# Performance work log

Hardware: AMD Instinct MI355X
Metric: run time of the kernel (lower is better)

The kernel has to match this reference:

```python
import jax, jax.numpy as jnp
import numpy as np

MARGIN = 5.0
NUM_CLASSES = 21


def setup_inputs() -> dict:
    key = jax.random.key(0)
    k1, k2, k3 = jax.random.split(key, 3)
    B, D, C = 65536, 512, NUM_CLASSES
    features = jax.random.normal(k1, (B, D), dtype=jnp.float32)
    centers = jax.random.normal(k2, (C, D), dtype=jnp.float32)
    labels = jax.random.randint(k3, (B,), 0, C, dtype=jnp.int64)
    return {"features": features, "centers": centers, "labels": labels}


def reference(features, centers, labels):
    # Halved squared euclidean distances, batch x num_classes, via the
    # ||f||^2 + ||c||^2 - 2 f.c expansion (avoids a B x C x D intermediate).
    f2 = jnp.sum(features * features, axis=1, keepdims=True)      # (B, 1)
    c2 = jnp.sum(centers * centers, axis=1)[None, :]              # (1, C)
    d = 0.5 * (f2 + c2 - 2.0 * (features @ centers.T))            # (B, C)

    B = features.shape[0]
    pos = d[jnp.arange(B), labels]                                 # dist to own center
    same = labels[:, None] == jnp.arange(NUM_CLASSES)[None, :]     # (B, C)
    neg = jnp.min(jnp.where(same, jnp.inf, d), axis=1)             # nearest other center
    loss = jnp.mean(jax.nn.relu(pos + MARGIN - neg))
    return loss
```

## Files before the change

### kernel.cpp

```cpp
#include <hip/hip_runtime.h>
#include <float.h>

#define DIM      512
#define NCLS     21
#define MARGIN_V 5.0f
#define ROWS_PB  64
#define DC       32
#define NSTAGE   (DIM / DC)
#define LPAD     (DC + 1)

__global__ __launch_bounds__(64)
void center_norm_kernel(const float* __restrict__ centers,
                        float* __restrict__ halfc2) {
    const int c = blockIdx.x;
    const int t = threadIdx.x;
    float s = 0.f;
#pragma unroll
    for (int i = 0; i < DIM / 64; ++i) {
        float v = centers[c * DIM + i * 64 + t];
        s = fmaf(v, v, s);
    }
#pragma unroll
    for (int off = 32; off > 0; off >>= 1)
        s += __shfl_down(s, off, 64);
    if (t == 0) halfc2[c] = 0.5f * s;
}

__global__ __launch_bounds__(64)
void tcl_main_kernel(const float* __restrict__ feat,
                     const float* __restrict__ centers,
                     const int* __restrict__ labels,
                     const float* __restrict__ halfc2,
                     float* __restrict__ out) {
    __shared__ float tile[ROWS_PB * LPAD];
    const int t    = threadIdx.x;
    const int row0 = blockIdx.x * ROWS_PB;

    const int lab = labels[row0 + t];

    float acc[NCLS];
#pragma unroll
    for (int c = 0; c < NCLS; ++c) acc[c] = 0.f;

    const float4* fbase = reinterpret_cast<const float4*>(feat);

    float4 pre[8];
#pragma unroll
    for (int i = 0; i < 8; ++i) {
        int f = i * 64 + t;
        int row = f >> 3, j4 = f & 7;
        pre[i] = fbase[(size_t)(row0 + row) * (DIM / 4) + j4];
    }

#pragma unroll 1
    for (int s = 0; s < NSTAGE; ++s) {
        __syncthreads();
#pragma unroll
        for (int i = 0; i < 8; ++i) {
            int f = i * 64 + t;
            int row = f >> 3, j4 = f & 7;
            int base = row * LPAD + j4 * 4;
            tile[base + 0] = pre[i].x;
            tile[base + 1] = pre[i].y;
            tile[base + 2] = pre[i].z;
            tile[base + 3] = pre[i].w;
        }
        __syncthreads();
        if (s + 1 < NSTAGE) {
#pragma unroll
            for (int i = 0; i < 8; ++i) {
                int f = i * 64 + t;
                int row = f >> 3, j4 = f & 7;
                pre[i] = fbase[(size_t)(row0 + row) * (DIM / 4)
                               + (size_t)(s + 1) * (DC / 4) + j4];
            }
        }
        const int dbase = s * DC;
#pragma unroll 2
        for (int jj = 0; jj < DC; jj += 4) {
            float f0 = tile[t * LPAD + jj + 0];
            float f1 = tile[t * LPAD + jj + 1];
            float f2 = tile[t * LPAD + jj + 2];
            float f3 = tile[t * LPAD + jj + 3];
#pragma unroll
            for (int c = 0; c < NCLS; ++c) {
                const float* cp = &centers[c * DIM + dbase + jj];
                acc[c] = fmaf(f0, cp[0],
                          fmaf(f1, cp[1],
                           fmaf(f2, cp[2],
                            fmaf(f3, cp[3], acc[c]))));
            }
        }
    }

    float pos = 0.f, neg = FLT_MAX;
#pragma unroll
    for (int c = 0; c < NCLS; ++c) {
        float e = halfc2[c] - acc[c];
        pos = (c == lab) ? e : pos;
        neg = (c == lab) ? neg : fminf(neg, e);
    }
    float v = fmaxf(pos + MARGIN_V - neg, 0.f);

#pragma unroll
    for (int off = 32; off > 0; off >>= 1)
        v += __shfl_down(v, off, 64);
    if (t == 0) atomicAdd(out, v * (1.0f / 65536.f));
}

extern "C" void kernel_launch(void* const* d_in, const int* in_sizes, int n_in,
                              void* d_out, int out_size, void* d_ws, size_t ws_size,
                              hipStream_t stream) {
    const float* feat    = (const float*)d_in[0];
    const float* centers = (const float*)d_in[1];
    const int*   labels  = (const int*)d_in[2];
    float* out    = (float*)d_out;
    float* halfc2 = (float*)d_ws;

    hipMemsetAsync(d_out, 0, (size_t)out_size * sizeof(float), stream);
    center_norm_kernel<<<NCLS, 64, 0, stream>>>(centers, halfc2);

    const int nblocks = 65536 / ROWS_PB;
    tcl_main_kernel<<<nblocks, 64, 0, stream>>>(feat, centers, labels, halfc2, out);
}
```

Measured before the change: 254.5 us.

## Split feature dimension across eight waves per block with LDS tree reduction

Each 64-row block now runs 8 waves, each handling a 64-wide slice of the 512 feature dimensions with its own private LDS tile, so no block-level barriers are needed in the main loop. Partial per-class dot products are combined with a three-step LDS tree reduction before wave 0 computes the loss. This raises parallelism per block and shortens each thread's serial K loop, and it uses more LDS and adds a reduction phase.

```diff
diff --git a/kernel.cpp b/kernel.cpp
--- a/kernel.cpp
+++ b/kernel.cpp
@@ -5,9 +5,13 @@
 #define NCLS     21
 #define MARGIN_V 5.0f
 #define ROWS_PB  64
-#define DC       32
-#define NSTAGE   (DIM / DC)
+#define NWAVES   8
+#define DSLICE   (DIM / NWAVES)
+#define DC       16
+#define NSTAGE   (DSLICE / DC)
 #define LPAD     (DC + 1)
+#define TILEF    (ROWS_PB * LPAD)
+#define CST      (NCLS + 1)
 
 __global__ __launch_bounds__(64)
 void center_norm_kernel(const float* __restrict__ centers,
@@ -26,62 +30,61 @@
     if (t == 0) halfc2[c] = 0.5f * s;
 }
 
-__global__ __launch_bounds__(64)
+__global__ __launch_bounds__(512, 8)
 void tcl_main_kernel(const float* __restrict__ feat,
                      const float* __restrict__ centers,
                      const int* __restrict__ labels,
                      const float* __restrict__ halfc2,
                      float* __restrict__ out) {
-    __shared__ float tile[ROWS_PB * LPAD];
-    const int t    = threadIdx.x;
+    __shared__ float lds[NWAVES * TILEF];
+
+    const int tid  = threadIdx.x;
+    const int w    = __builtin_amdgcn_readfirstlane(tid >> 6);
+    const int t    = tid & 63;
     const int row0 = blockIdx.x * ROWS_PB;
 
-    const int lab = labels[row0 + t];
+    float* mytile = &lds[w * TILEF];
 
     float acc[NCLS];
 #pragma unroll
     for (int c = 0; c < NCLS; ++c) acc[c] = 0.f;
 
     const float4* fbase = reinterpret_cast<const float4*>(feat);
+    const int rsub = t >> 2;
+    const int j4   = t & 3;
+    const size_t gbase = (size_t)(row0 + rsub) * (DIM / 4)
+                       + (size_t)w * (DSLICE / 4) + j4;
 
-    float4 pre[8];
+    float4 pre[4];
 #pragma unroll
-    for (int i = 0; i < 8; ++i) {
-        int f = i * 64 + t;
-        int row = f >> 3, j4 = f & 7;
-        pre[i] = fbase[(size_t)(row0 + row) * (DIM / 4) + j4];
-    }
+    for (int i = 0; i < 4; ++i)
+        pre[i] = fbase[gbase + (size_t)i * 16 * (DIM / 4)];
+
+    const int wbase = rsub * LPAD + j4 * 4;
 
 #pragma unroll 1
     for (int s = 0; s < NSTAGE; ++s) {
-        __syncthreads();
 #pragma unroll
-        for (int i = 0; i < 8; ++i) {
-            int f = i * 64 + t;
-            int row = f >> 3, j4 = f & 7;
-            int base = row * LPAD + j4 * 4;
-            tile[base + 0] = pre[i].x;
-            tile[base + 1] = pre[i].y;
-            tile[base + 2] = pre[i].z;
-            tile[base + 3] = pre[i].w;
+        for (int i = 0; i < 4; ++i) {
+            int b = i * 16 * LPAD + wbase;
+            mytile[b + 0] = pre[i].x;
+            mytile[b + 1] = pre[i].y;
+            mytile[b + 2] = pre[i].z;
+            mytile[b + 3] = pre[i].w;
         }
-        __syncthreads();
         if (s + 1 < NSTAGE) {
 #pragma unroll
-            for (int i = 0; i < 8; ++i) {
-                int f = i * 64 + t;
-                int row = f >> 3, j4 = f & 7;
-                pre[i] = fbase[(size_t)(row0 + row) * (DIM / 4)
-                               + (size_t)(s + 1) * (DC / 4) + j4];
-            }
+            for (int i = 0; i < 4; ++i)
+                pre[i] = fbase[gbase + (size_t)i * 16 * (DIM / 4)
+                               + (size_t)(s + 1) * (DC / 4)];
         }
-        const int dbase = s * DC;
+        const int dbase = w * DSLICE + s * DC;
 #pragma unroll 2
         for (int jj = 0; jj < DC; jj += 4) {
-            float f0 = tile[t * LPAD + jj + 0];
-            float f1 = tile[t * LPAD + jj + 1];
-            float f2 = tile[t * LPAD + jj + 2];
-            float f3 = tile[t * LPAD + jj + 3];
+            float f0 = mytile[t * LPAD + jj + 0];
+            float f1 = mytile[t * LPAD + jj + 1];
+            float f2 = mytile[t * LPAD + jj + 2];
+            float f3 = mytile[t * LPAD + jj + 3];
 #pragma unroll
             for (int c = 0; c < NCLS; ++c) {
                 const float* cp = &centers[c * DIM + dbase + jj];
@@ -93,19 +96,54 @@
         }
     }
 
-    float pos = 0.f, neg = FLT_MAX;
+    float* comb = lds;
+    __syncthreads();
+    if (w >= 4) {
+        float* p = &comb[((w - 4) * ROWS_PB + t) * CST];
 #pragma unroll
-    for (int c = 0; c < NCLS; ++c) {
-        float e = halfc2[c] - acc[c];
-        pos = (c == lab) ? e : pos;
-        neg = (c == lab) ? neg : fminf(neg, e);
+        for (int c = 0; c < NCLS; ++c) p[c] = acc[c];
     }
-    float v = fmaxf(pos + MARGIN_V - neg, 0.f);
-
+    __syncthreads();
+    if (w < 4) {
+        const float* p = &comb[(w * ROWS_PB + t) * CST];
 #pragma unroll
-    for (int off = 32; off > 0; off >>= 1)
-        v += __shfl_down(v, off, 64);
-    if (t == 0) atomicAdd(out, v * (1.0f / 65536.f));
+        for (int c = 0; c < NCLS; ++c) acc[c] += p[c];
+    }
+    __syncthreads();
+    if (w == 2 || w == 3) {
+        float* p = &comb[((w - 2) * ROWS_PB + t) * CST];
+#pragma unroll
+        for (int c = 0; c < NCLS; ++c) p[c] = acc[c];
+    }
+    __syncthreads();
+    if (w < 2) {
+        const float* p = &comb[(w * ROWS_PB + t) * CST];
+#pragma unroll
+        for (int c = 0; c < NCLS; ++c) acc[c] += p[c];
+    }
+    __syncthreads();
+    if (w == 1) {
+        float* p = &comb[t * CST];
+#pragma unroll
+        for (int c = 0; c < NCLS; ++c) p[c] = acc[c];
+    }
+    __syncthreads();
+    if (w == 0) {
+        const float* p = &comb[t * CST];
+        const int lab = labels[row0 + t];
+        float pos = 0.f, neg = FLT_MAX;
+#pragma unroll
+        for (int c = 0; c < NCLS; ++c) {
+            float e = halfc2[c] - (acc[c] + p[c]);
+            pos = (c == lab) ? e : pos;
+            neg = (c == lab) ? neg : fminf(neg, e);
+        }
+        float v = fmaxf(pos + MARGIN_V - neg, 0.f);
+#pragma unroll
+        for (int off = 32; off > 0; off >>= 1)
+            v += __shfl_down(v, off, 64);
+        if (t == 0) atomicAdd(out, v * (1.0f / 65536.f));
+    }
 }
 
 extern "C" void kernel_launch(void* const* d_in, const int* in_sizes, int n_in,
@@ -121,5 +159,5 @@
     center_norm_kernel<<<NCLS, 64, 0, stream>>>(centers, halfc2);
 
     const int nblocks = 65536 / ROWS_PB;
-    tcl_main_kernel<<<nblocks, 64, 0, stream>>>(feat, centers, labels, halfc2, out);
+    tcl_main_kernel<<<nblocks, 512, 0, stream>>>(feat, centers, labels, halfc2, out);
 }
```

After: 209.0 us. 17.9% less time.
